# Performance work log

Measured on AMD Instinct MI355X. Metric: run time of the kernel, lower is better.

## Reference

```python
import jax, jax.numpy as jnp
import numpy as np

N, E, G = 50000, 800000, 100
H, C = 4, 64


def _gatv2(x, src, dst, ea, Wl, bl, Wr, br, We, att, bias):
    # PyG GATv2Conv: x_l = lin_l(x) (source side), x_r = lin_r(x) (target side)
    xl = (x @ Wl + bl).reshape(-1, H, C)
    xr = (x @ Wr + br).reshape(-1, H, C)
    e = (ea @ We).reshape(-1, H, C)               # [E,H,C]
    m = jax.nn.leaky_relu(xl[src] + xr[dst] + e, negative_slope=0.2)
    alpha = jnp.einsum('ehc,hc->eh', m, att)      # [E,H]
    amax = jax.ops.segment_max(alpha, dst, num_segments=N)
    amax = jnp.where(jnp.isfinite(amax), amax, jnp.float32(0.0))
    ex = jnp.exp(alpha - amax[dst])
    denom = jax.ops.segment_sum(ex, dst, num_segments=N)
    a = ex / (denom[dst] + jnp.float32(1e-16))    # segment softmax over in-edges
    out = jax.ops.segment_sum(xl[src] * a[..., None], dst, num_segments=N)
    return out.reshape(N, H * C) + bias


def setup_inputs() -> dict:
    key = jax.random.key(0)
    ks = jax.random.split(key, 24)
    lin = lambda k, i, o: (jax.random.normal(k, (i, o), jnp.float32) / np.sqrt(i).astype(np.float32))
    x = jax.random.normal(ks[0], (N, 8), jnp.float32)
    edge_index = jnp.stack([jax.random.randint(ks[1], (E,), 0, N),
                            jax.random.randint(ks[2], (E,), 0, N)])
    edge_attr = jax.random.normal(ks[3], (E, 1), jnp.float32)
    batch = jnp.sort(jax.random.randint(ks[4], (N,), 0, G))
    return dict(
        x=x, edge_index=edge_index, edge_attr=edge_attr, batch=batch,
        enc_W=lin(ks[5], 8, 64), enc_b=jnp.zeros((64,), jnp.float32),
        g1_Wl=lin(ks[6], 64, 256), g1_bl=jnp.zeros((256,), jnp.float32),
        g1_Wr=lin(ks[7], 64, 256), g1_br=jnp.zeros((256,), jnp.float32),
        g1_We=lin(ks[8], 1, 256),
        g1_att=jax.random.normal(ks[9], (H, C), jnp.float32) / np.sqrt(C).astype(np.float32),
        g1_bias=jnp.zeros((256,), jnp.float32),
        g2_Wl=lin(ks[10], 256, 256), g2_bl=jnp.zeros((256,), jnp.float32),
        g2_Wr=lin(ks[11], 256, 256), g2_br=jnp.zeros((256,), jnp.float32),
        g2_We=lin(ks[12], 1, 256),
        g2_att=jax.random.normal(ks[13], (H, C), jnp.float32) / np.sqrt(C).astype(np.float32),
        g2_bias=jnp.zeros((256,), jnp.float32),
        p1_W=lin(ks[14], 256, 128), p1_b=jnp.zeros((128,), jnp.float32),
        ln_g=jnp.ones((128,), jnp.float32), ln_b=jnp.zeros((128,), jnp.float32),
        p2_W=lin(ks[15], 128, 64), p2_b=jnp.zeros((64,), jnp.float32),
    )


def reference(x, edge_index, edge_attr, batch,
              enc_W, enc_b,
              g1_Wl, g1_bl, g1_Wr, g1_br, g1_We, g1_att, g1_bias,
              g2_Wl, g2_bl, g2_Wr, g2_br, g2_We, g2_att, g2_bias,
              p1_W, p1_b, ln_g, ln_b, p2_W, p2_b):
    src, dst = edge_index[0], edge_index[1]
    h = jax.nn.relu(x @ enc_W + enc_b)
    h = jax.nn.relu(_gatv2(h, src, dst, edge_attr, g1_Wl, g1_bl, g1_Wr, g1_br, g1_We, g1_att, g1_bias))
    h = jax.nn.relu(_gatv2(h, src, dst, edge_attr, g2_Wl, g2_bl, g2_Wr, g2_br, g2_We, g2_att, g2_bias))
    # global mean pool over graphs
    sums = jax.ops.segment_sum(h, batch, num_segments=G)
    cnt = jax.ops.segment_sum(jnp.ones((N, 1), h.dtype), batch, num_segments=G)
    p = sums / jnp.maximum(cnt, jnp.float32(1.0))
    # post MLP (dropout is identity in eval)
    z = p @ p1_W + p1_b
    mu = jnp.mean(z, axis=-1, keepdims=True)
    var = jnp.mean(jnp.square(z - mu), axis=-1, keepdims=True)
    z = (z - mu) * jax.lax.rsqrt(var + jnp.float32(1e-5)) * ln_g + ln_b
    z = jax.nn.relu(z)
    return jax.nn.relu(z @ p2_W + p2_b)
```

## Files before the change

### kernel.cpp

```cpp
#include <hip/hip_runtime.h>

#define NH 4
#define CH 64

__device__ __forceinline__ float bf2f(unsigned short u) {
  return __uint_as_float(((unsigned)u) << 16);
}
__device__ __forceinline__ unsigned short f2bf(float f) {
  unsigned b = __float_as_uint(f);
  return (unsigned short)((b + 0x7fffu + ((b >> 16) & 1u)) >> 16);
}

__global__ void encoder_kernel(const float* __restrict__ x, const float* __restrict__ W,
                               const float* __restrict__ b, float* __restrict__ h, int N) {
  int idx = blockIdx.x * blockDim.x + threadIdx.x;
  if (idx >= N * 64) return;
  int n = idx >> 6, j = idx & 63;
  const float* xp = x + n * 8;
  float acc = b[j];
#pragma unroll
  for (int k = 0; k < 8; ++k) acc = fmaf(xp[k], W[k * 64 + j], acc);
  h[idx] = fmaxf(acc, 0.0f);
}

template <int K>
__global__ void lin_lr_kernel(const float* __restrict__ h,
                              const float* __restrict__ Wl, const float* __restrict__ bl,
                              const float* __restrict__ Wr, const float* __restrict__ br,
                              unsigned short* __restrict__ xlb, float* __restrict__ xr, int N) {
  __shared__ float hs[8][K];
  int n0 = blockIdx.x * 8;
  int j = threadIdx.x;
  int nmax = N - n0; if (nmax > 8) nmax = 8;
  for (int idx = j; idx < nmax * K; idx += 256) {
    int m = idx / K, k = idx % K;
    hs[m][k] = h[(size_t)(n0 + m) * K + k];
  }
  __syncthreads();
  float accl[8], accr[8];
  float bjl = bl[j], bjr = br[j];
#pragma unroll
  for (int m = 0; m < 8; ++m) { accl[m] = bjl; accr[m] = bjr; }
  for (int k = 0; k < K; ++k) {
    float wl = Wl[k * 256 + j];
    float wr = Wr[k * 256 + j];
#pragma unroll
    for (int m = 0; m < 8; ++m) {
      accl[m] = fmaf(hs[m][k], wl, accl[m]);
      accr[m] = fmaf(hs[m][k], wr, accr[m]);
    }
  }
  for (int m = 0; m < nmax; ++m) {
    xlb[(size_t)(n0 + m) * 256 + j] = f2bf(accl[m]);
    xr[(size_t)(n0 + m) * 256 + j] = accr[m];
  }
}

__global__ void hist_kernel(const int* __restrict__ dst, int* __restrict__ deg, int E) {
  int e = blockIdx.x * blockDim.x + threadIdx.x;
  if (e < E) atomicAdd(&deg[dst[e]], 1);
}

__global__ void scan_partial_kernel(const int* __restrict__ deg, int* __restrict__ partial, int N) {
  __shared__ int sm[256];
  int t = threadIdx.x;
  int i = blockIdx.x * 256 + t;
  sm[t] = (i < N) ? deg[i] : 0;
  __syncthreads();
#pragma unroll
  for (int s = 128; s > 0; s >>= 1) {
    if (t < s) sm[t] += sm[t + s];
    __syncthreads();
  }
  if (t == 0) partial[blockIdx.x] = sm[0];
}

__global__ void scan_offsets_kernel(int* __restrict__ partial, int nb) {
  __shared__ int sm[256];
  int t = threadIdx.x;
  int v = (t < nb) ? partial[t] : 0;
  sm[t] = v;
  __syncthreads();
#pragma unroll
  for (int off = 1; off < 256; off <<= 1) {
    int a = (t >= off) ? sm[t - off] : 0;
    __syncthreads();
    sm[t] += a;
    __syncthreads();
  }
  if (t < nb) partial[t] = sm[t] - v;
}

__global__ void scan_final_kernel(const int* __restrict__ deg, const int* __restrict__ partial,
                                  int* __restrict__ rowptr, int* __restrict__ cursor, int N, int E) {
  __shared__ int sm[256];
  int t = threadIdx.x;
  int i = blockIdx.x * 256 + t;
  int v = (i < N) ? deg[i] : 0;
  sm[t] = v;
  __syncthreads();
#pragma unroll
  for (int off = 1; off < 256; off <<= 1) {
    int a = (t >= off) ? sm[t - off] : 0;
    __syncthreads();
    sm[t] += a;
    __syncthreads();
  }
  if (i < N) {
    int ex = partial[blockIdx.x] + sm[t] - v;
    rowptr[i] = ex;
    cursor[i] = ex;
  }
  if (i == 0) rowptr[N] = E;
}

__global__ void scatter_build_kernel(const int* __restrict__ src, const int* __restrict__ dst,
                                     const float* __restrict__ ea, int* __restrict__ cursor,
                                     int2* __restrict__ edg, int E) {
  int e = blockIdx.x * blockDim.x + threadIdx.x;
  if (e >= E) return;
  int d = dst[e];
  int pos = atomicAdd(&cursor[d], 1);
  edg[pos] = make_int2(src[e], __float_as_int(ea[e]));
}

__device__ __forceinline__ void edge_accum(const ushort4 xu, const float eav,
                                           const float4 xr4, const float4 We4, const float4 at4,
                                           float4& acc, float& denom) {
  float4 xlv;
  xlv.x = bf2f(xu.x); xlv.y = bf2f(xu.y); xlv.z = bf2f(xu.z); xlv.w = bf2f(xu.w);
  float4 v;
  v.x = fmaf(eav, We4.x, xlv.x + xr4.x);
  v.y = fmaf(eav, We4.y, xlv.y + xr4.y);
  v.z = fmaf(eav, We4.z, xlv.z + xr4.z);
  v.w = fmaf(eav, We4.w, xlv.w + xr4.w);
  v.x = (v.x >= 0.f) ? v.x : 0.2f * v.x;
  v.y = (v.y >= 0.f) ? v.y : 0.2f * v.y;
  v.z = (v.z >= 0.f) ? v.z : 0.2f * v.z;
  v.w = (v.w >= 0.f) ? v.w : 0.2f * v.w;
  float p = v.x * at4.x + v.y * at4.y + v.z * at4.z + v.w * at4.w;
  p += __shfl_xor(p, 1, 64);
  p += __shfl_xor(p, 2, 64);
  p += __shfl_xor(p, 4, 64);
  p += __shfl_xor(p, 8, 64);
  float ex = __expf(p);
  denom += ex;
  acc.x = fmaf(ex, xlv.x, acc.x);
  acc.y = fmaf(ex, xlv.y, acc.y);
  acc.z = fmaf(ex, xlv.z, acc.z);
  acc.w = fmaf(ex, xlv.w, acc.w);
}

template <bool POOL>
__global__ void gat_aggregate_kernel(const int* __restrict__ rowptr,
                                     const int2* __restrict__ edg,
                                     const unsigned short* __restrict__ xlb,
                                     const float* __restrict__ xr,
                                     const float* __restrict__ We,
                                     const float* __restrict__ att,
                                     const float* __restrict__ bias,
                                     float* __restrict__ out,
                                     const int* __restrict__ batch,
                                     float* __restrict__ sums,
                                     float* __restrict__ cnt,
                                     int N) {
  int d = (int)((blockIdx.x * (size_t)blockDim.x + threadIdx.x) >> 6);
  int lane = threadIdx.x & 63;
  if (d >= N) return;
  const ushort4* xlp = (const ushort4*)xlb;
  float4 xr4 = ((const float4*)xr)[(size_t)d * 64 + lane];
  float4 We4 = ((const float4*)We)[lane];
  float4 at4 = ((const float4*)att)[lane];
  int beg = rowptr[d], end = rowptr[d + 1];
  float4 acc = {0.f, 0.f, 0.f, 0.f};
  float denom = 0.f;
  int i = beg;
  for (; i + 7 < end; i += 8) {
    int2 e0 = edg[i], e1 = edg[i + 1], e2 = edg[i + 2], e3 = edg[i + 3];
    int2 e4 = edg[i + 4], e5 = edg[i + 5], e6 = edg[i + 6], e7 = edg[i + 7];
    ushort4 a0 = xlp[(size_t)e0.x * 64 + lane];
    ushort4 a1 = xlp[(size_t)e1.x * 64 + lane];
    ushort4 a2 = xlp[(size_t)e2.x * 64 + lane];
    ushort4 a3 = xlp[(size_t)e3.x * 64 + lane];
    ushort4 a4 = xlp[(size_t)e4.x * 64 + lane];
    ushort4 a5 = xlp[(size_t)e5.x * 64 + lane];
    ushort4 a6 = xlp[(size_t)e6.x * 64 + lane];
    ushort4 a7 = xlp[(size_t)e7.x * 64 + lane];
    edge_accum(a0, __int_as_float(e0.y), xr4, We4, at4, acc, denom);
    edge_accum(a1, __int_as_float(e1.y), xr4, We4, at4, acc, denom);
    edge_accum(a2, __int_as_float(e2.y), xr4, We4, at4, acc, denom);
    edge_accum(a3, __int_as_float(e3.y), xr4, We4, at4, acc, denom);
    edge_accum(a4, __int_as_float(e4.y), xr4, We4, at4, acc, denom);
    edge_accum(a5, __int_as_float(e5.y), xr4, We4, at4, acc, denom);
    edge_accum(a6, __int_as_float(e6.y), xr4, We4, at4, acc, denom);
    edge_accum(a7, __int_as_float(e7.y), xr4, We4, at4, acc, denom);
  }
  for (; i + 1 < end; i += 2) {
    int2 e0 = edg[i], e1 = edg[i + 1];
    ushort4 a0 = xlp[(size_t)e0.x * 64 + lane];
    ushort4 a1 = xlp[(size_t)e1.x * 64 + lane];
    edge_accum(a0, __int_as_float(e0.y), xr4, We4, at4, acc, denom);
    edge_accum(a1, __int_as_float(e1.y), xr4, We4, at4, acc, denom);
  }
  if (i < end) {
    int2 e0 = edg[i];
    ushort4 a0 = xlp[(size_t)e0.x * 64 + lane];
    edge_accum(a0, __int_as_float(e0.y), xr4, We4, at4, acc, denom);
  }
  float inv = 1.f / (denom + 1e-16f);
  float4 b4 = ((const float4*)bias)[lane];
  float4 o;
  o.x = fmaxf(fmaf(acc.x, inv, b4.x), 0.f);
  o.y = fmaxf(fmaf(acc.y, inv, b4.y), 0.f);
  o.z = fmaxf(fmaf(acc.z, inv, b4.z), 0.f);
  o.w = fmaxf(fmaf(acc.w, inv, b4.w), 0.f);
  if (POOL) {
    int g = batch[d];
    float* sg = sums + (size_t)g * 256 + lane * 4;
    atomicAdd(sg + 0, o.x);
    atomicAdd(sg + 1, o.y);
    atomicAdd(sg + 2, o.z);
    atomicAdd(sg + 3, o.w);
    if (lane == 0) atomicAdd(&cnt[g], 1.0f);
  } else {
    ((float4*)out)[(size_t)d * 64 + lane] = o;
  }
}

__global__ void mlp_kernel(const float* __restrict__ sums, const float* __restrict__ cnt,
                           const float* __restrict__ p1W, const float* __restrict__ p1b,
                           const float* __restrict__ lng, const float* __restrict__ lnb,
                           const float* __restrict__ p2W, const float* __restrict__ p2b,
                           float* __restrict__ outp, int G) {
  __shared__ float p[256];
  __shared__ float z[128];
  __shared__ float wsum[2];
  __shared__ float wsum2[2];
  int g = blockIdx.x;
  int t = threadIdx.x;
  float c = fmaxf(cnt[g], 1.0f);
  p[t] = sums[(size_t)g * 256 + t] / c;
  p[t + 128] = sums[(size_t)g * 256 + t + 128] / c;
  __syncthreads();
  float acc = p1b[t];
  for (int k = 0; k < 256; ++k) acc = fmaf(p[k], p1W[k * 128 + t], acc);
  float v = acc;
#pragma unroll
  for (int off = 32; off > 0; off >>= 1) v += __shfl_xor(v, off, 64);
  if ((t & 63) == 0) wsum[t >> 6] = v;
  __syncthreads();
  float mu = (wsum[0] + wsum[1]) * (1.0f / 128.0f);
  float dv = acc - mu;
  float vv = dv * dv;
#pragma unroll
  for (int off = 32; off > 0; off >>= 1) vv += __shfl_xor(vv, off, 64);
  if ((t & 63) == 0) wsum2[t >> 6] = vv;
  __syncthreads();
  float var = (wsum2[0] + wsum2[1]) * (1.0f / 128.0f);
  float zv = dv * rsqrtf(var + 1e-5f) * lng[t] + lnb[t];
  z[t] = fmaxf(zv, 0.0f);
  __syncthreads();
  if (t < 64) {
    float o = p2b[t];
    for (int k = 0; k < 128; ++k) o = fmaf(z[k], p2W[k * 64 + t], o);
    outp[(size_t)g * 64 + t] = fmaxf(o, 0.0f);
  }
}

extern "C" void kernel_launch(void* const* d_in, const int* in_sizes, int n_in,
                              void* d_out, int out_size, void* d_ws, size_t ws_size,
                              hipStream_t stream) {
  const float* x      = (const float*)d_in[0];
  const int*   ei     = (const int*)d_in[1];
  const float* ea     = (const float*)d_in[2];
  const int*   batch  = (const int*)d_in[3];
  const float* enc_W  = (const float*)d_in[4];
  const float* enc_b  = (const float*)d_in[5];
  const float* Wl1    = (const float*)d_in[6];
  const float* bl1    = (const float*)d_in[7];
  const float* Wr1    = (const float*)d_in[8];
  const float* br1    = (const float*)d_in[9];
  const float* We1    = (const float*)d_in[10];
  const float* att1   = (const float*)d_in[11];
  const float* bias1  = (const float*)d_in[12];
  const float* Wl2    = (const float*)d_in[13];
  const float* bl2    = (const float*)d_in[14];
  const float* Wr2    = (const float*)d_in[15];
  const float* br2    = (const float*)d_in[16];
  const float* We2    = (const float*)d_in[17];
  const float* att2   = (const float*)d_in[18];
  const float* bias2  = (const float*)d_in[19];
  const float* p1W    = (const float*)d_in[20];
  const float* p1b    = (const float*)d_in[21];
  const float* lng    = (const float*)d_in[22];
  const float* lnb    = (const float*)d_in[23];
  const float* p2W    = (const float*)d_in[24];
  const float* p2b    = (const float*)d_in[25];
  float* outp = (float*)d_out;

  int N = in_sizes[0] / 8;
  int E = in_sizes[2];
  int G = out_size / 64;
  const int* src = ei;
  const int* dst = ei + E;
  int nb = (N + 255) / 256;

  float* ws      = (float*)d_ws;
  float* h0      = ws;
  float* B1      = h0     + (size_t)N * 64;
  float* B2      = B1     + (size_t)N * 256;
  float* sums    = B2     + (size_t)N * 256;
  float* cnt     = sums   + (size_t)G * 256;
  unsigned short* xlb = (unsigned short*)(cnt + G);
  int2*  edg     = (int2*)(xlb + (size_t)N * 256);
  int*   rowptr  = (int*)(edg + (size_t)E);
  int*   cursor  = rowptr + (size_t)(N + 1);
  int*   partial = cursor + (size_t)N;

  encoder_kernel<<<(N * 64 + 255) / 256, 256, 0, stream>>>(x, enc_W, enc_b, h0, N);

  hipMemsetAsync(cursor, 0, (size_t)N * sizeof(int), stream);
  hist_kernel<<<(E + 255) / 256, 256, 0, stream>>>(dst, cursor, E);
  scan_partial_kernel<<<nb, 256, 0, stream>>>(cursor, partial, N);
  scan_offsets_kernel<<<1, 256, 0, stream>>>(partial, nb);
  scan_final_kernel<<<nb, 256, 0, stream>>>(cursor, partial, rowptr, cursor, N, E);
  scatter_build_kernel<<<(E + 255) / 256, 256, 0, stream>>>(src, dst, ea, cursor, edg, E);

  lin_lr_kernel<64><<<(N + 7) / 8, 256, 0, stream>>>(h0, Wl1, bl1, Wr1, br1, xlb, B1, N);
  gat_aggregate_kernel<false><<<(N + 3) / 4, 256, 0, stream>>>(
      rowptr, edg, xlb, B1, We1, att1, bias1, B2, nullptr, nullptr, nullptr, N);

  lin_lr_kernel<256><<<(N + 7) / 8, 256, 0, stream>>>(B2, Wl2, bl2, Wr2, br2, xlb, B1, N);
  hipMemsetAsync(sums, 0, ((size_t)G * 256 + G) * sizeof(float), stream);
  gat_aggregate_kernel<true><<<(N + 3) / 4, 256, 0, stream>>>(
      rowptr, edg, xlb, B1, We2, att2, bias2, nullptr, batch, sums, cnt, N);

  mlp_kernel<<<G, 128, 0, stream>>>(sums, cnt, p1W, p1b, lng, lnb, p2W, p2b, outp, G);
}
```

Measured before the change: 1.053 ms.

## Split wavefront into two half-waves each processing separate edges with 8 channels per lane

Restructures the GATv2 aggregation so each lane handles 8 channels through 16-byte bf16 loads, and the two 32-lane halves of a wavefront work on different edges at once. The halves' partial softmax denominators and accumulators are combined with a cross-half shuffle at the end. This raises memory-level parallelism per gather and cuts one shuffle step per edge, at the cost of more registers per lane and idle lanes on odd tails and in the epilogue.

```diff
diff --git a/kernel.cpp b/kernel.cpp
--- a/kernel.cpp
+++ b/kernel.cpp
@@ -3,9 +3,6 @@
 #define NH 4
 #define CH 64
 
-__device__ __forceinline__ float bf2f(unsigned short u) {
-  return __uint_as_float(((unsigned)u) << 16);
-}
 __device__ __forceinline__ unsigned short f2bf(float f) {
   unsigned b = __float_as_uint(f);
   return (unsigned short)((b + 0x7fffu + ((b >> 16) & 1u)) >> 16);
@@ -124,31 +121,28 @@
   edg[pos] = make_int2(src[e], __float_as_int(ea[e]));
 }
 
-__device__ __forceinline__ void edge_accum(const ushort4 xu, const float eav,
-                                           const float4 xr4, const float4 We4, const float4 at4,
-                                           float4& acc, float& denom) {
-  float4 xlv;
-  xlv.x = bf2f(xu.x); xlv.y = bf2f(xu.y); xlv.z = bf2f(xu.z); xlv.w = bf2f(xu.w);
-  float4 v;
-  v.x = fmaf(eav, We4.x, xlv.x + xr4.x);
-  v.y = fmaf(eav, We4.y, xlv.y + xr4.y);
-  v.z = fmaf(eav, We4.z, xlv.z + xr4.z);
-  v.w = fmaf(eav, We4.w, xlv.w + xr4.w);
-  v.x = (v.x >= 0.f) ? v.x : 0.2f * v.x;
-  v.y = (v.y >= 0.f) ? v.y : 0.2f * v.y;
-  v.z = (v.z >= 0.f) ? v.z : 0.2f * v.z;
-  v.w = (v.w >= 0.f) ? v.w : 0.2f * v.w;
-  float p = v.x * at4.x + v.y * at4.y + v.z * at4.z + v.w * at4.w;
+__device__ __forceinline__ void edge_accum8(const uint4 q, const float eav,
+                                            const float* xr8, const float* We8, const float* at8,
+                                            float* acc, float& denom) {
+  float xl[8];
+  xl[0] = __uint_as_float(q.x << 16); xl[1] = __uint_as_float(q.x & 0xffff0000u);
+  xl[2] = __uint_as_float(q.y << 16); xl[3] = __uint_as_float(q.y & 0xffff0000u);
+  xl[4] = __uint_as_float(q.z << 16); xl[5] = __uint_as_float(q.z & 0xffff0000u);
+  xl[6] = __uint_as_float(q.w << 16); xl[7] = __uint_as_float(q.w & 0xffff0000u);
+  float p = 0.f;
+#pragma unroll
+  for (int k = 0; k < 8; ++k) {
+    float v = fmaf(eav, We8[k], xl[k] + xr8[k]);
+    v = (v >= 0.f) ? v : 0.2f * v;
+    p = fmaf(v, at8[k], p);
+  }
   p += __shfl_xor(p, 1, 64);
   p += __shfl_xor(p, 2, 64);
   p += __shfl_xor(p, 4, 64);
-  p += __shfl_xor(p, 8, 64);
   float ex = __expf(p);
   denom += ex;
-  acc.x = fmaf(ex, xlv.x, acc.x);
-  acc.y = fmaf(ex, xlv.y, acc.y);
-  acc.z = fmaf(ex, xlv.z, acc.z);
-  acc.w = fmaf(ex, xlv.w, acc.w);
+#pragma unroll
+  for (int k = 0; k < 8; ++k) acc[k] = fmaf(ex, xl[k], acc[k]);
 }
 
 template <bool POOL>
@@ -167,63 +161,70 @@
   int d = (int)((blockIdx.x * (size_t)blockDim.x + threadIdx.x) >> 6);
   int lane = threadIdx.x & 63;
   if (d >= N) return;
-  const ushort4* xlp = (const ushort4*)xlb;
-  float4 xr4 = ((const float4*)xr)[(size_t)d * 64 + lane];
-  float4 We4 = ((const float4*)We)[lane];
-  float4 at4 = ((const float4*)att)[lane];
+  int half = lane >> 5;
+  int sl = lane & 31;
+  int c0 = sl * 8;
+
+  const uint4* xlp = (const uint4*)xlb;
+  float xr8[8], We8[8], at8[8];
+  {
+    float4 a = *(const float4*)(xr + (size_t)d * 256 + c0);
+    float4 b = *(const float4*)(xr + (size_t)d * 256 + c0 + 4);
+    xr8[0]=a.x; xr8[1]=a.y; xr8[2]=a.z; xr8[3]=a.w; xr8[4]=b.x; xr8[5]=b.y; xr8[6]=b.z; xr8[7]=b.w;
+    a = *(const float4*)(We + c0); b = *(const float4*)(We + c0 + 4);
+    We8[0]=a.x; We8[1]=a.y; We8[2]=a.z; We8[3]=a.w; We8[4]=b.x; We8[5]=b.y; We8[6]=b.z; We8[7]=b.w;
+    a = *(const float4*)(att + c0); b = *(const float4*)(att + c0 + 4);
+    at8[0]=a.x; at8[1]=a.y; at8[2]=a.z; at8[3]=a.w; at8[4]=b.x; at8[5]=b.y; at8[6]=b.z; at8[7]=b.w;
+  }
   int beg = rowptr[d], end = rowptr[d + 1];
-  float4 acc = {0.f, 0.f, 0.f, 0.f};
+  float acc[8] = {0.f,0.f,0.f,0.f,0.f,0.f,0.f,0.f};
   float denom = 0.f;
   int i = beg;
-  for (; i + 7 < end; i += 8) {
-    int2 e0 = edg[i], e1 = edg[i + 1], e2 = edg[i + 2], e3 = edg[i + 3];
-    int2 e4 = edg[i + 4], e5 = edg[i + 5], e6 = edg[i + 6], e7 = edg[i + 7];
-    ushort4 a0 = xlp[(size_t)e0.x * 64 + lane];
-    ushort4 a1 = xlp[(size_t)e1.x * 64 + lane];
-    ushort4 a2 = xlp[(size_t)e2.x * 64 + lane];
-    ushort4 a3 = xlp[(size_t)e3.x * 64 + lane];
-    ushort4 a4 = xlp[(size_t)e4.x * 64 + lane];
-    ushort4 a5 = xlp[(size_t)e5.x * 64 + lane];
-    ushort4 a6 = xlp[(size_t)e6.x * 64 + lane];
-    ushort4 a7 = xlp[(size_t)e7.x * 64 + lane];
-    edge_accum(a0, __int_as_float(e0.y), xr4, We4, at4, acc, denom);
-    edge_accum(a1, __int_as_float(e1.y), xr4, We4, at4, acc, denom);
-    edge_accum(a2, __int_as_float(e2.y), xr4, We4, at4, acc, denom);
-    edge_accum(a3, __int_as_float(e3.y), xr4, We4, at4, acc, denom);
-    edge_accum(a4, __int_as_float(e4.y), xr4, We4, at4, acc, denom);
-    edge_accum(a5, __int_as_float(e5.y), xr4, We4, at4, acc, denom);
-    edge_accum(a6, __int_as_float(e6.y), xr4, We4, at4, acc, denom);
-    edge_accum(a7, __int_as_float(e7.y), xr4, We4, at4, acc, denom);
+  for (; i + 3 < end; i += 4) {
+    int2 ea_ = edg[i + half];
+    int2 eb_ = edg[i + 2 + half];
+    uint4 qa = xlp[(size_t)ea_.x * 32 + sl];
+    uint4 qb = xlp[(size_t)eb_.x * 32 + sl];
+    edge_accum8(qa, __int_as_float(ea_.y), xr8, We8, at8, acc, denom);
+    edge_accum8(qb, __int_as_float(eb_.y), xr8, We8, at8, acc, denom);
   }
   for (; i + 1 < end; i += 2) {
-    int2 e0 = edg[i], e1 = edg[i + 1];
-    ushort4 a0 = xlp[(size_t)e0.x * 64 + lane];
-    ushort4 a1 = xlp[(size_t)e1.x * 64 + lane];
-    edge_accum(a0, __int_as_float(e0.y), xr4, We4, at4, acc, denom);
-    edge_accum(a1, __int_as_float(e1.y), xr4, We4, at4, acc, denom);
-  }
-  if (i < end) {
-    int2 e0 = edg[i];
-    ushort4 a0 = xlp[(size_t)e0.x * 64 + lane];
-    edge_accum(a0, __int_as_float(e0.y), xr4, We4, at4, acc, denom);
-  }
+    int2 ea_ = edg[i + half];
+    uint4 qa = xlp[(size_t)ea_.x * 32 + sl];
+    edge_accum8(qa, __int_as_float(ea_.y), xr8, We8, at8, acc, denom);
+  }
+  if (i < end && half == 0) {
+    int2 ea_ = edg[i];
+    uint4 qa = xlp[(size_t)ea_.x * 32 + sl];
+    edge_accum8(qa, __int_as_float(ea_.y), xr8, We8, at8, acc, denom);
+  }
+  denom += __shfl_xor(denom, 32, 64);
+#pragma unroll
+  for (int k = 0; k < 8; ++k) acc[k] += __shfl_xor(acc[k], 32, 64);
   float inv = 1.f / (denom + 1e-16f);
-  float4 b4 = ((const float4*)bias)[lane];
-  float4 o;
-  o.x = fmaxf(fmaf(acc.x, inv, b4.x), 0.f);
-  o.y = fmaxf(fmaf(acc.y, inv, b4.y), 0.f);
-  o.z = fmaxf(fmaf(acc.z, inv, b4.z), 0.f);
-  o.w = fmaxf(fmaf(acc.w, inv, b4.w), 0.f);
-  if (POOL) {
-    int g = batch[d];
-    float* sg = sums + (size_t)g * 256 + lane * 4;
-    atomicAdd(sg + 0, o.x);
-    atomicAdd(sg + 1, o.y);
-    atomicAdd(sg + 2, o.z);
-    atomicAdd(sg + 3, o.w);
-    if (lane == 0) atomicAdd(&cnt[g], 1.0f);
-  } else {
-    ((float4*)out)[(size_t)d * 64 + lane] = o;
+  if (half == 0) {
+    float4 b0 = *(const float4*)(bias + c0);
+    float4 b1 = *(const float4*)(bias + c0 + 4);
+    float o[8];
+    o[0] = fmaxf(fmaf(acc[0], inv, b0.x), 0.f);
+    o[1] = fmaxf(fmaf(acc[1], inv, b0.y), 0.f);
+    o[2] = fmaxf(fmaf(acc[2], inv, b0.z), 0.f);
+    o[3] = fmaxf(fmaf(acc[3], inv, b0.w), 0.f);
+    o[4] = fmaxf(fmaf(acc[4], inv, b1.x), 0.f);
+    o[5] = fmaxf(fmaf(acc[5], inv, b1.y), 0.f);
+    o[6] = fmaxf(fmaf(acc[6], inv, b1.z), 0.f);
+    o[7] = fmaxf(fmaf(acc[7], inv, b1.w), 0.f);
+    if (POOL) {
+      int g = batch[d];
+      float* sg = sums + (size_t)g * 256 + c0;
+#pragma unroll
+      for (int k = 0; k < 8; ++k) atomicAdd(sg + k, o[k]);
+      if (sl == 0) atomicAdd(&cnt[g], 1.0f);
+    } else {
+      float* op = out + (size_t)d * 256 + c0;
+      *(float4*)op = make_float4(o[0], o[1], o[2], o[3]);
+      *(float4*)(op + 4) = make_float4(o[4], o[5], o[6], o[7]);
+    }
   }
 }
 
```

Measured after the change: 1.252 ms. 1.19x slower.
